# Kernel optimization log

Measured on AMD Instinct MI355X. Metric: run time of the kernel, lower is better.

Reference implementation:

```python
import math
import jax, jax.numpy as jnp
import numpy as np

B, SEQ, N_EMBD, N_HEAD, MAX_LEN = 2, 2048, 1024, 16, 2048
D_HEAD = N_EMBD // N_HEAD


def setup_inputs() -> dict:
    key = jax.random.key(0)
    k0, k1, k2, k3, k4 = jax.random.split(key, 5)
    x = jax.random.normal(k0, (B, SEQ, N_EMBD), jnp.float32)
    # nn.Linear weights stored [out_features, in_features]; scale ~ kaiming-ish
    s = 1.0 / math.sqrt(N_EMBD)
    Wq = jax.random.normal(k1, (N_EMBD, N_EMBD), jnp.float32) * s
    Wk = jax.random.normal(k2, (N_EMBD, N_EMBD), jnp.float32) * s
    Wv = jax.random.normal(k3, (N_EMBD, N_EMBD), jnp.float32) * s
    Er = jax.random.normal(k4, (MAX_LEN, D_HEAD), jnp.float32)
    return {"x": x, "Wq": Wq, "Wk": Wk, "Wv": Wv, "Er": Er}


def _skew(QEr):
    # QEr: [B, H, S, S]; mask with anti-diagonal tril-flip, then pad/reshape skew
    S = QEr.shape[-1]
    anti = jnp.flip(jnp.tril(jnp.ones((S, S), QEr.dtype)), axis=1)
    QEr = QEr * anti  # masked_fill(mask==0, 0)
    padded = jnp.pad(QEr, ((0, 0), (0, 0), (0, 0), (1, 0)))  # [B,H,S,S+1]
    Bq, H, S_, Sp1 = padded.shape
    return padded.reshape(Bq, H, Sp1, S_)[:, :, 1:, :]  # [B,H,S,S]


def reference(x, Wq, Wk, Wv, Er):
    Bx, S, E = x.shape
    H, d = N_HEAD, D_HEAD

    def proj(W):
        return jnp.einsum('bse,fe->bsf', x, W).reshape(Bx, S, H, d).transpose(0, 2, 1, 3)

    q, k, v = proj(Wq), proj(Wk), proj(Wv)  # [B,H,S,d]
    qk = jnp.einsum('bhqd,bhkd->bhqk', q, k)
    Er_s = Er[MAX_LEN - S:, :]  # [S, d]
    QEr = jnp.einsum('bhqd,rd->bhqr', q, Er_s)  # [B,H,S,S]
    Srel = _skew(QEr)
    attn = (qk + Srel) / math.sqrt(d)
    causal = jnp.tril(jnp.ones((S, S), bool))
    attn = jnp.where(causal, attn, -jnp.inf)
    p = jax.nn.softmax(attn, axis=-1)
    out = jnp.einsum('bhqk,bhkd->bhqd', p, v)
    return out.transpose(0, 2, 1, 3).reshape(Bx, S, E)
```

## Files before the change

kernel.cpp:

```cpp
#include <hip/hip_runtime.h>
#include <hip/hip_bf16.h>
#include <stdint.h>

#define S_LEN 2048
#define EMB   1024
#define NH    16
#define DH    64
#define BATCH 2

typedef short bf16x8 __attribute__((ext_vector_type(8)));
typedef short bf16x4 __attribute__((ext_vector_type(4)));
typedef float f32x4  __attribute__((ext_vector_type(4)));

__device__ __forceinline__ unsigned short f2bf(float f) {
    union { float f; unsigned int u; } v; v.f = f;
    unsigned int r = v.u + 0x7FFFu + ((v.u >> 16) & 1u);
    return (unsigned short)(r >> 16);
}

__device__ __forceinline__ bf16x8 load8f_to_bf(const float* __restrict__ p) {
    const float4* p4 = (const float4*)p;
    float4 x0 = p4[0];
    float4 x1 = p4[1];
    bf16x8 r;
    r[0] = (short)f2bf(x0.x); r[1] = (short)f2bf(x0.y);
    r[2] = (short)f2bf(x0.z); r[3] = (short)f2bf(x0.w);
    r[4] = (short)f2bf(x1.x); r[5] = (short)f2bf(x1.y);
    r[6] = (short)f2bf(x1.z); r[7] = (short)f2bf(x1.w);
    return r;
}

__device__ __forceinline__ void bar_lds() {
    asm volatile("s_waitcnt lgkmcnt(0)" ::: "memory");
    __builtin_amdgcn_sched_barrier(0);
    __builtin_amdgcn_s_barrier();
    __builtin_amdgcn_sched_barrier(0);
}

__device__ __forceinline__ void gload_lds16(const unsigned short* g, unsigned short* l) {
    __builtin_amdgcn_global_load_lds(
        (const __attribute__((address_space(1))) unsigned int*)g,
        (__attribute__((address_space(3))) unsigned int*)l, 16, 0, 0);
}

__global__ __launch_bounds__(256) void cvt_bf16(
    const float* __restrict__ x,  const float* __restrict__ wq,
    const float* __restrict__ wk, const float* __restrict__ wv,
    const float* __restrict__ er,
    unsigned short* __restrict__ xb, unsigned short* __restrict__ wb,
    unsigned short* __restrict__ erb)
{
    const int NX = 4194304 / 8, NW = 1048576 / 8, NE = 131072 / 8;
    const int total = NX + 3 * NW + NE;
    for (int i8 = blockIdx.x * 256 + threadIdx.x; i8 < total; i8 += gridDim.x * 256) {
        const float* src; unsigned short* dst; int off;
        if      (i8 < NX)          { src = x;  dst = xb;            off = i8; }
        else if (i8 < NX + NW)     { src = wq; dst = wb;            off = i8 - NX; }
        else if (i8 < NX + 2 * NW) { src = wk; dst = wb + 1048576;  off = i8 - NX - NW; }
        else if (i8 < NX + 3 * NW) { src = wv; dst = wb + 2097152;  off = i8 - NX - 2 * NW; }
        else                       { src = er; dst = erb;           off = i8 - NX - 3 * NW; }
        ((bf16x8*)dst)[off] = load8f_to_bf(src + (size_t)off * 8);
    }
}

__global__ __launch_bounds__(256) void proj_kernel_bf(
    const unsigned short* __restrict__ xb, const unsigned short* __restrict__ wb,
    unsigned short* __restrict__ Qb, unsigned short* __restrict__ Kb,
    unsigned short* __restrict__ Vt)
{
    __shared__ __align__(16) unsigned short Al[128 * 64];
    __shared__ __align__(16) unsigned short Bl[128 * 64];

    const int tid  = threadIdx.x;
    const int lane = tid & 63;
    const int w    = tid >> 6;
    const int wr   = w >> 1;
    const int wc   = w & 1;
    const int m0   = blockIdx.x * 128;
    const int c0   = blockIdx.y * 128;
    const int wsel = c0 >> 10;
    const int f0   = c0 & 1023;
    const unsigned short* __restrict__ W = wb + (size_t)wsel * 1048576;

    const int lr = lane & 15;
    const int g  = lane >> 4;

    const int srow8 = tid >> 3;
    const int scol  = (((tid & 7) ^ (srow8 & 7))) * 8;

    f32x4 acc[4][4];
#pragma unroll
    for (int i = 0; i < 4; i++)
#pragma unroll
        for (int n = 0; n < 4; n++) acc[i][n] = (f32x4){0.f, 0.f, 0.f, 0.f};

    for (int k0 = 0; k0 < 1024; k0 += 64) {
        __syncthreads();
#pragma unroll
        for (int i = 0; i < 4; i++) {
            gload_lds16(&xb[(size_t)(m0 + i * 32 + srow8) * 1024 + k0 + scol],
                        &Al[(i * 4 + w) * 512]);
            gload_lds16(&W [(size_t)(f0 + i * 32 + srow8) * 1024 + k0 + scol],
                        &Bl[(i * 4 + w) * 512]);
        }
        __syncthreads();

#pragma unroll
        for (int kk = 0; kk < 2; kk++) {
            bf16x8 a[4], b[4];
#pragma unroll
            for (int i = 0; i < 4; i++) {
                int ar = wr * 64 + i * 16 + lr;
                a[i] = *(const bf16x8*)&Al[ar * 64 + (((kk * 4 + g) ^ (ar & 7)) * 8)];
            }
#pragma unroll
            for (int n = 0; n < 4; n++) {
                int br = wc * 64 + n * 16 + lr;
                b[n] = *(const bf16x8*)&Bl[br * 64 + (((kk * 4 + g) ^ (br & 7)) * 8)];
            }
#pragma unroll
            for (int i = 0; i < 4; i++)
#pragma unroll
                for (int n = 0; n < 4; n++)
                    acc[i][n] = __builtin_amdgcn_mfma_f32_16x16x32_bf16(a[i], b[n], acc[i][n], 0, 0, 0);
        }
    }

#pragma unroll
    for (int i = 0; i < 4; i++) {
#pragma unroll
        for (int n = 0; n < 4; n++) {
#pragma unroll
            for (int j = 0; j < 4; j++) {
                int row_m = m0 + wr * 64 + i * 16 + g * 4 + j;
                int c     = c0 + wc * 64 + n * 16 + lr;
                int f     = c & 1023;
                int h     = f >> 6;
                int dd    = f & 63;
                int bb    = row_m >> 11;
                int s     = row_m & 2047;
                int bh    = bb * 16 + h;
                unsigned short bv = f2bf(acc[i][n][j]);
                if (wsel == 0)      Qb[((size_t)bh * 2048 + s) * 64 + dd] = bv;
                else if (wsel == 1) Kb[((size_t)bh * 2048 + s) * 64 + dd] = bv;
                else                Vt[((size_t)bh * 64 + dd) * 2048 + s] = bv;
            }
        }
    }
}

__global__ __launch_bounds__(256) void proj_kernel_f32(
    const float* __restrict__ x,
    const float* __restrict__ Wq, const float* __restrict__ Wk,
    const float* __restrict__ Wv,
    unsigned short* __restrict__ Qb, unsigned short* __restrict__ Kb,
    unsigned short* __restrict__ Vt)
{
    const int tid  = threadIdx.x;
    const int lane = tid & 63;
    const int w    = tid >> 6;
    const int wr   = w >> 1;
    const int wc   = w & 1;
    const int m0   = blockIdx.x * 128 + wr * 64;
    const int c0   = blockIdx.y * 128 + wc * 64;
    const int wsel = c0 >> 10;
    const int f0   = c0 & 1023;
    const float* __restrict__ W = (wsel == 0) ? Wq : (wsel == 1) ? Wk : Wv;

    const int lr = lane & 15;
    const int lk = (lane >> 4) * 8;

    f32x4 acc[4][4];
#pragma unroll
    for (int i = 0; i < 4; i++)
#pragma unroll
        for (int n = 0; n < 4; n++) acc[i][n] = (f32x4){0.f, 0.f, 0.f, 0.f};

    for (int k0 = 0; k0 < 1024; k0 += 32) {
        bf16x8 a[4], b[4];
#pragma unroll
        for (int i = 0; i < 4; i++)
            a[i] = load8f_to_bf(&x[(size_t)(m0 + i * 16 + lr) * 1024 + k0 + lk]);
#pragma unroll
        for (int n = 0; n < 4; n++)
            b[n] = load8f_to_bf(&W[(size_t)(f0 + n * 16 + lr) * 1024 + k0 + lk]);
#pragma unroll
        for (int i = 0; i < 4; i++)
#pragma unroll
            for (int n = 0; n < 4; n++)
                acc[i][n] = __builtin_amdgcn_mfma_f32_16x16x32_bf16(a[i], b[n], acc[i][n], 0, 0, 0);
    }

    const int g = lane >> 4;
#pragma unroll
    for (int i = 0; i < 4; i++) {
#pragma unroll
        for (int n = 0; n < 4; n++) {
#pragma unroll
            for (int j = 0; j < 4; j++) {
                int row_m = m0 + i * 16 + g * 4 + j;
                int c     = c0 + n * 16 + lr;
                int f     = c & 1023;
                int h     = f >> 6;
                int dd    = f & 63;
                int bb    = row_m >> 11;
                int s     = row_m & 2047;
                int bh    = bb * 16 + h;
                unsigned short bv = f2bf(acc[i][n][j]);
                if (wsel == 0)      Qb[((size_t)bh * 2048 + s) * 64 + dd] = bv;
                else if (wsel == 1) Kb[((size_t)bh * 2048 + s) * 64 + dd] = bv;
                else                Vt[((size_t)bh * 64 + dd) * 2048 + s] = bv;
            }
        }
    }
}

__global__ void cvt_er(const float* __restrict__ Er, unsigned short* __restrict__ Erb, int n)
{
    int i = blockIdx.x * 256 + threadIdx.x;
    if (i < n) Erb[i] = f2bf(Er[i]);
}

__global__ __launch_bounds__(256) void attn_kernel(
    const unsigned short* __restrict__ Qb, const unsigned short* __restrict__ Kb,
    const unsigned short* __restrict__ Vt, const unsigned short* __restrict__ Erb,
    float* __restrict__ out)
{
    __shared__ __align__(16) unsigned short Kl[64 * 64];
    __shared__ __align__(16) unsigned short Vl[64 * 64];
    __shared__ __align__(16) unsigned short El[128 * 64];
    __shared__ __align__(16) float          Rt[4][80][18];

    const int tid  = threadIdx.x;
    const int lane = tid & 63;
    const int w    = tid >> 6;

    const int i0  = blockIdx.x;
    const int xcd = i0 & 7;
    const int b2  = (i0 >> 3) & 3;
    const int qt  = 31 - (i0 >> 5);
    const int bh  = (xcd << 2) | b2;

    const int lr = lane & 15;
    const int g  = lane >> 4;
    const int lk = g * 8;

    const unsigned short* __restrict__ Qrow = Qb + (size_t)bh * 2048 * 64;
    const unsigned short* __restrict__ Krow = Kb + (size_t)bh * 2048 * 64;
    const unsigned short* __restrict__ Vrow = Vt + (size_t)bh * 64 * 2048;

    const float SCL = 0.125f * 1.44269504089f;
    const int bb  = bh >> 4;
    const int h   = bh & 15;
    const int q0  = qt * 64;
    const int q0w = q0 + w * 16;
    const int eoff = 48 - 16 * w;

    bf16x8 aq[2];
#pragma unroll
    for (int kk = 0; kk < 2; kk++)
        aq[kk] = *(const bf16x8*)&Qrow[(size_t)(q0w + lr) * 64 + kk * 32 + lk];

    f32x4 o[4];
#pragma unroll
    for (int m = 0; m < 4; m++) o[m] = (f32x4){0.f, 0.f, 0.f, 0.f};
    float mrow = -1e30f, lsum = 0.f;

    bf16x8 sk[2], sv[2], se[4];
    auto stage_load = [&](int kt) {
        const int k0  = kt * 64;
        const int rbT = 2047 + k0 - q0 - 63;
#pragma unroll
        for (int i = 0; i < 2; i++) {
            int c = i * 256 + tid, kr = c >> 3, o8 = (c & 7) * 8;
            sk[i] = *(const bf16x8*)&Krow[(size_t)(k0 + kr) * 64 + o8];
        }
#pragma unroll
        for (int i = 0; i < 2; i++) {
            int c = i * 256 + tid, d = c >> 3, o8 = (c & 7) * 8;
            sv[i] = *(const bf16x8*)&Vrow[(size_t)d * 2048 + k0 + o8];
        }
#pragma unroll
        for (int i = 0; i < 4; i++) {
            int c = i * 256 + tid, wr_ = c >> 3, o8 = (c & 7) * 8;
            int rr = rbT + wr_; rr = rr > 2047 ? 2047 : rr;
            se[i] = *(const bf16x8*)&Erb[(size_t)rr * 64 + o8];
        }
    };
    auto stage_write = [&]() {
#pragma unroll
        for (int i = 0; i < 2; i++) {
            int c = i * 256 + tid, kr = c >> 3, o8 = (c & 7) * 8;
            *(bf16x8*)&Kl[(kr * 64 + o8) ^ ((kr & 7) << 3)] = sk[i];
        }
#pragma unroll
        for (int i = 0; i < 2; i++) {
            int c = i * 256 + tid, d = c >> 3, o8 = (c & 7) * 8;
            *(bf16x8*)&Vl[(d * 64 + o8) ^ ((d & 7) << 3)] = sv[i];
        }
#pragma unroll
        for (int i = 0; i < 4; i++) {
            int c = i * 256 + tid, wr_ = c >> 3, o8 = (c & 7) * 8;
            *(bf16x8*)&El[(wr_ * 64 + o8) ^ ((wr_ & 7) << 3)] = se[i];
        }
    };

    stage_load(0);

#pragma unroll 1
    for (int kt = 0; kt <= qt; ++kt) {
        const int k0 = kt * 64;

        bar_lds();
        stage_write();
        if (kt < qt) stage_load(kt + 1);
        bar_lds();

        f32x4 s[4], r[5];
#pragma unroll
        for (int n = 0; n < 4; n++) s[n] = (f32x4){0.f, 0.f, 0.f, 0.f};
#pragma unroll
        for (int n = 0; n < 5; n++) r[n] = (f32x4){0.f, 0.f, 0.f, 0.f};
#pragma unroll
        for (int kk = 0; kk < 2; kk++) {
            bf16x8 kb[4], be[5];
#pragma unroll
            for (int n = 0; n < 4; n++) {
                int kr = n * 16 + lr;
                kb[n] = *(const bf16x8*)&Kl[(kr * 64 + kk * 32 + lk) ^ ((kr & 7) << 3)];
            }
#pragma unroll
            for (int n = 0; n < 5; n++) {
                int er = eoff + n * 16 + lr;
                be[n] = *(const bf16x8*)&El[(er * 64 + kk * 32 + lk) ^ ((er & 7) << 3)];
            }
#pragma unroll
            for (int n = 0; n < 4; n++)
                s[n] = __builtin_amdgcn_mfma_f32_16x16x32_bf16(kb[n], aq[kk], s[n], 0, 0, 0);
#pragma unroll
            for (int n = 0; n < 5; n++)
                r[n] = __builtin_amdgcn_mfma_f32_16x16x32_bf16(be[n], aq[kk], r[n], 0, 0, 0);
        }

#pragma unroll
        for (int n = 0; n < 5; n++)
#pragma unroll
            for (int j = 0; j < 4; j++)
                Rt[w][n * 16 + g * 4 + j][lr] = r[n][j];

        bar_lds();

        float pmax = -1e30f;
#pragma unroll
        for (int n = 0; n < 4; n++) {
#pragma unroll
            for (int j = 0; j < 4; j++) {
                int wd = n * 16 + g * 4 + j + 15 - lr;
                float sc = (s[n][j] + Rt[w][wd][lr]) * SCL;
                if (k0 + n * 16 + g * 4 + j > q0w + lr) sc = -1e30f;
                s[n][j] = sc;
                pmax = fmaxf(pmax, sc);
            }
        }

        if (__any(pmax > mrow + 4.0f)) {
            pmax = fmaxf(pmax, __shfl_xor(pmax, 16));
            pmax = fmaxf(pmax, __shfl_xor(pmax, 32));
            float mn   = fmaxf(mrow, pmax);
            float corr = exp2f(mrow - mn);
            mrow = mn;
            lsum *= corr;
#pragma unroll
            for (int j = 0; j < 4; j++) {
                float cj = __shfl(corr, g * 4 + j);
#pragma unroll
                for (int m = 0; m < 4; m++) o[m][j] *= cj;
            }
        }

        float rs = 0.f;
        bf16x4 pa[4];
#pragma unroll
        for (int n = 0; n < 4; n++)
#pragma unroll
            for (int j = 0; j < 4; j++) {
                float pv = exp2f(s[n][j] - mrow);
                rs += pv;
                pa[n][j] = (short)f2bf(pv);
            }
        lsum += rs;

#pragma unroll
        for (int m = 0; m < 4; m++) {
#pragma unroll
            for (int n = 0; n < 4; n++) {
                int d = 16 * m + lr;
                bf16x4 vb = *(const bf16x4*)&Vl[(d * 64 + 16 * n + 4 * g) ^ ((d & 7) << 3)];
                o[m] = __builtin_amdgcn_mfma_f32_16x16x16bf16_1k(pa[n], vb, o[m], 0, 0, 0);
            }
        }
    }

    float ls = lsum;
    ls += __shfl_xor(ls, 16);
    ls += __shfl_xor(ls, 32);
    float linv = 1.0f / ls;
#pragma unroll
    for (int j = 0; j < 4; j++) {
        float lj = __shfl(linv, g * 4 + j);
#pragma unroll
        for (int m = 0; m < 4; m++) {
            int row = q0w + g * 4 + j;
            int col = h * 64 + 16 * m + lr;
            out[((size_t)bb * 2048 + row) * 1024 + col] = o[m][j] * lj;
        }
    }
}

extern "C" void kernel_launch(void* const* d_in, const int* in_sizes, int n_in,
                              void* d_out, int out_size, void* d_ws, size_t ws_size,
                              hipStream_t stream)
{
    const float* x  = (const float*)d_in[0];
    const float* Wq = (const float*)d_in[1];
    const float* Wk = (const float*)d_in[2];
    const float* Wv = (const float*)d_in[3];
    const float* Er = (const float*)d_in[4];
    float* out = (float*)d_out;

    char* ws = (char*)d_ws;
    const size_t MB = 1024 * 1024;
    unsigned short* Qb  = (unsigned short*)(ws);
    unsigned short* Kb  = (unsigned short*)(ws + 8  * MB);
    unsigned short* Vt  = (unsigned short*)(ws + 16 * MB);
    unsigned short* Erb = (unsigned short*)(ws + 24 * MB);
    unsigned short* xb  = (unsigned short*)(ws + 25 * MB);
    unsigned short* wb  = (unsigned short*)(ws + 33 * MB);

    if (ws_size >= (size_t)39 * MB) {
        cvt_bf16<<<dim3(1024), dim3(256), 0, stream>>>(x, Wq, Wk, Wv, Er, xb, wb, Erb);
        proj_kernel_bf<<<dim3(32, 24), dim3(256), 0, stream>>>(xb, wb, Qb, Kb, Vt);
    } else {
        cvt_er<<<dim3(512), dim3(256), 0, stream>>>(Er, Erb, 2048 * 64);
        proj_kernel_f32<<<dim3(32, 24), dim3(256), 0, stream>>>(x, Wq, Wk, Wv, Qb, Kb, Vt);
    }
    attn_kernel<<<dim3(1024), dim3(256), 0, stream>>>(Qb, Kb, Vt, Erb, out);
}
```

Measured before the change: 140.4 us.

## Reuse overlapping Er rows via ring buffer, split causal mask path, add setprio

Consecutive key tiles need Er windows that overlap by 64 rows. The Er tile in LDS becomes a 128-row ring buffer, so each iteration loads only 64 new Er rows instead of 128, which halves Er global traffic and LDS writes. The causal mask compare now runs only on the diagonal tile. MFMA sections are wrapped in s_setprio and the bf16 conversion switches to the HIP intrinsic. These are several independent micro-optimizations, and the ring indexing adds a little address arithmetic.

Measured after the change: 130.3 us. 7.2% less time.

```diff
diff --git a/kernel.cpp b/kernel.cpp
--- a/kernel.cpp
+++ b/kernel.cpp
@@ -16,6 +16,11 @@
     union { float f; unsigned int u; } v; v.f = f;
     unsigned int r = v.u + 0x7FFFu + ((v.u >> 16) & 1u);
     return (unsigned short)(r >> 16);
+}
+
+__device__ __forceinline__ short f2bf_fast(float f) {
+    __hip_bfloat16 h = __float2bfloat16(f);
+    return *reinterpret_cast<short*>(&h);
 }
 
 __device__ __forceinline__ bf16x8 load8f_to_bf(const float* __restrict__ p) {
@@ -255,6 +260,7 @@
     const int q0  = qt * 64;
     const int q0w = q0 + w * 16;
     const int eoff = 48 - 16 * w;
+    const int rbT0 = 1984 - q0;
 
     bf16x8 aq[2];
 #pragma unroll
@@ -267,53 +273,82 @@
     float mrow = -1e30f, lsum = 0.f;
 
     bf16x8 sk[2], sv[2], se[4];
-    auto stage_load = [&](int kt) {
-        const int k0  = kt * 64;
-        const int rbT = 2047 + k0 - q0 - 63;
-#pragma unroll
-        for (int i = 0; i < 2; i++) {
-            int c = i * 256 + tid, kr = c >> 3, o8 = (c & 7) * 8;
-            sk[i] = *(const bf16x8*)&Krow[(size_t)(k0 + kr) * 64 + o8];
-        }
-#pragma unroll
-        for (int i = 0; i < 2; i++) {
-            int c = i * 256 + tid, d = c >> 3, o8 = (c & 7) * 8;
-            sv[i] = *(const bf16x8*)&Vrow[(size_t)d * 2048 + k0 + o8];
-        }
+    const int o8u = (tid & 7) * 8;
+
+    auto kv_load = [&](int kt) {
+        const int k0 = kt * 64;
+#pragma unroll
+        for (int i = 0; i < 2; i++) {
+            int kr = ((i * 256 + tid) >> 3);
+            sk[i] = *(const bf16x8*)&Krow[(size_t)(k0 + kr) * 64 + o8u];
+        }
+#pragma unroll
+        for (int i = 0; i < 2; i++) {
+            int d = ((i * 256 + tid) >> 3);
+            sv[i] = *(const bf16x8*)&Vrow[(size_t)d * 2048 + k0 + o8u];
+        }
+    };
+    auto kv_write = [&]() {
+#pragma unroll
+        for (int i = 0; i < 2; i++) {
+            int kr = ((i * 256 + tid) >> 3);
+            *(bf16x8*)&Kl[(kr * 64 + o8u) ^ ((kr & 7) << 3)] = sk[i];
+        }
+#pragma unroll
+        for (int i = 0; i < 2; i++) {
+            int d = ((i * 256 + tid) >> 3);
+            *(bf16x8*)&Vl[(d * 64 + o8u) ^ ((d & 7) << 3)] = sv[i];
+        }
+    };
+    auto e_load4 = [&](int base) {
 #pragma unroll
         for (int i = 0; i < 4; i++) {
-            int c = i * 256 + tid, wr_ = c >> 3, o8 = (c & 7) * 8;
-            int rr = rbT + wr_; rr = rr > 2047 ? 2047 : rr;
-            se[i] = *(const bf16x8*)&Erb[(size_t)rr * 64 + o8];
-        }
-    };
-    auto stage_write = [&]() {
-#pragma unroll
-        for (int i = 0; i < 2; i++) {
-            int c = i * 256 + tid, kr = c >> 3, o8 = (c & 7) * 8;
-            *(bf16x8*)&Kl[(kr * 64 + o8) ^ ((kr & 7) << 3)] = sk[i];
-        }
-#pragma unroll
-        for (int i = 0; i < 2; i++) {
-            int c = i * 256 + tid, d = c >> 3, o8 = (c & 7) * 8;
-            *(bf16x8*)&Vl[(d * 64 + o8) ^ ((d & 7) << 3)] = sv[i];
-        }
+            int r = base + ((i * 256 + tid) >> 3);
+            int rr = r > 2047 ? 2047 : r;
+            se[i] = *(const bf16x8*)&Erb[(size_t)rr * 64 + o8u];
+        }
+    };
+    auto e_load2 = [&](int base) {
+#pragma unroll
+        for (int i = 0; i < 2; i++) {
+            int r = base + ((i * 256 + tid) >> 3);
+            int rr = r > 2047 ? 2047 : r;
+            se[i] = *(const bf16x8*)&Erb[(size_t)rr * 64 + o8u];
+        }
+    };
+    auto e_write4 = [&](int base) {
 #pragma unroll
         for (int i = 0; i < 4; i++) {
-            int c = i * 256 + tid, wr_ = c >> 3, o8 = (c & 7) * 8;
-            *(bf16x8*)&El[(wr_ * 64 + o8) ^ ((wr_ & 7) << 3)] = se[i];
-        }
-    };
-
-    stage_load(0);
+            int r = base + ((i * 256 + tid) >> 3);
+            int slot = r & 127;
+            *(bf16x8*)&El[(slot * 64 + o8u) ^ ((slot & 7) << 3)] = se[i];
+        }
+    };
+    auto e_write2 = [&](int base) {
+#pragma unroll
+        for (int i = 0; i < 2; i++) {
+            int r = base + ((i * 256 + tid) >> 3);
+            int slot = r & 127;
+            *(bf16x8*)&El[(slot * 64 + o8u) ^ ((slot & 7) << 3)] = se[i];
+        }
+    };
+
+    kv_load(0);
+    e_load4(rbT0);
 
 #pragma unroll 1
     for (int kt = 0; kt <= qt; ++kt) {
         const int k0 = kt * 64;
+        const int ep = ((qt ^ kt ^ 1) & 1) << 6;
 
         bar_lds();
-        stage_write();
-        if (kt < qt) stage_load(kt + 1);
+        kv_write();
+        if (kt == 0) e_write4(rbT0);
+        else         e_write2(rbT0 + 64 * kt + 64);
+        if (kt < qt) {
+            kv_load(kt + 1);
+            e_load2(rbT0 + 64 * kt + 128);
+        }
         bar_lds();
 
         f32x4 s[4], r[5];
@@ -321,6 +356,7 @@
         for (int n = 0; n < 4; n++) s[n] = (f32x4){0.f, 0.f, 0.f, 0.f};
 #pragma unroll
         for (int n = 0; n < 5; n++) r[n] = (f32x4){0.f, 0.f, 0.f, 0.f};
+        __builtin_amdgcn_s_setprio(1);
 #pragma unroll
         for (int kk = 0; kk < 2; kk++) {
             bf16x8 kb[4], be[5];
@@ -331,7 +367,7 @@
             }
 #pragma unroll
             for (int n = 0; n < 5; n++) {
-                int er = eoff + n * 16 + lr;
+                int er = (eoff + n * 16 + lr + ep) & 127;
                 be[n] = *(const bf16x8*)&El[(er * 64 + kk * 32 + lk) ^ ((er & 7) << 3)];
             }
 #pragma unroll
@@ -341,6 +377,7 @@
             for (int n = 0; n < 5; n++)
                 r[n] = __builtin_amdgcn_mfma_f32_16x16x32_bf16(be[n], aq[kk], r[n], 0, 0, 0);
         }
+        __builtin_amdgcn_s_setprio(0);
 
 #pragma unroll
         for (int n = 0; n < 5; n++)
@@ -351,16 +388,28 @@
         bar_lds();
 
         float pmax = -1e30f;
-#pragma unroll
-        for (int n = 0; n < 4; n++) {
-#pragma unroll
-            for (int j = 0; j < 4; j++) {
-                int wd = n * 16 + g * 4 + j + 15 - lr;
-                float sc = (s[n][j] + Rt[w][wd][lr]) * SCL;
-                if (k0 + n * 16 + g * 4 + j > q0w + lr) sc = -1e30f;
-                s[n][j] = sc;
-                pmax = fmaxf(pmax, sc);
-            }
+        if (kt != qt) {
+#pragma unroll
+            for (int n = 0; n < 4; n++)
+#pragma unroll
+                for (int j = 0; j < 4; j++) {
+                    int wd = n * 16 + g * 4 + j + 15 - lr;
+                    float sc = (s[n][j] + Rt[w][wd][lr]) * SCL;
+                    s[n][j] = sc;
+                    pmax = fmaxf(pmax, sc);
+                }
+        } else {
+#pragma unroll
+            for (int n = 0; n < 4; n++)
+#pragma unroll
+                for (int j = 0; j < 4; j++) {
+                    int kl = n * 16 + g * 4 + j;
+                    int wd = kl + 15 - lr;
+                    float sc = (s[n][j] + Rt[w][wd][lr]) * SCL;
+                    if (kl > w * 16 + lr) sc = -1e30f;
+                    s[n][j] = sc;
+                    pmax = fmaxf(pmax, sc);
+                }
         }
 
         if (__any(pmax > mrow + 4.0f)) {
@@ -386,10 +435,11 @@
             for (int j = 0; j < 4; j++) {
                 float pv = exp2f(s[n][j] - mrow);
                 rs += pv;
-                pa[n][j] = (short)f2bf(pv);
+                pa[n][j] = f2bf_fast(pv);
             }
         lsum += rs;
 
+        __builtin_amdgcn_s_setprio(1);
 #pragma unroll
         for (int m = 0; m < 4; m++) {
 #pragma unroll
@@ -399,6 +449,7 @@
                 o[m] = __builtin_amdgcn_mfma_f32_16x16x16bf16_1k(pa[n], vb, o[m], 0, 0, 0);
             }
         }
+        __builtin_amdgcn_s_setprio(0);
     }
 
     float ls = lsum;
```
